# Performance work log

Hardware: AMD Instinct MI355X
Metric: run time of the kernel (lower is better)

Reference implementation:

```python
import jax, jax.numpy as jnp
import numpy as np
from jax import lax

B, C, N, NB = 64, 512, 1024, 4
BC = C // NB
KS = [3, 5, 7, 9]
LEVEL = 2  # min(2, pywt.dwt_max_level(1024, 8)) = 2
FL = 8  # db4 filter length
DN = ('NCH', 'OIH', 'NCH')
# pywt db4 decomposition filters
DEC_LO = jnp.array([-0.010597401784997278, 0.032883011666982945, 0.030841381835986965,
                    -0.18703481171888114, -0.02798376941698385, 0.6308807679295904,
                    0.7148465705525415, 0.23037781330885523], jnp.float32)
DEC_HI = jnp.array([-0.23037781330885523, 0.7148465705525415, -0.6308807679295904,
                    -0.02798376941698385, 0.18703481171888114, 0.030841381835986965,
                    -0.032883011666982945, -0.010597401784997278], jnp.float32)


def conv1d(x, w, b, pad):
    y = lax.conv_general_dilated(x, w, (1,), [(pad, pad)], dimension_numbers=DN)
    return y + b[None, :, None]


def bn_relu(x, g, beta, eps=1e-5):
    # BatchNorm1d in train mode: batch statistics over (B, L) per channel
    mu = x.mean(axis=(0, 2), keepdims=True)
    var = ((x - mu) ** 2).mean(axis=(0, 2), keepdims=True)
    xn = (x - mu) * lax.rsqrt(var + eps)
    return jax.nn.relu(xn * g[None, :, None] + beta[None, :, None])


def dwt1d(x):
    # single-level pywt-compatible DWT, symmetric mode. x: [B, C, n]
    b, c, n = x.shape
    out = (n + FL - 1) // 2
    p = 2 * (out - 1) - n + FL
    xp = jnp.pad(x, ((0, 0), (0, 0), (p // 2, p - p // 2)), mode='symmetric')
    k = jnp.stack([DEC_LO[::-1], DEC_HI[::-1]])[:, None, :]  # [2,1,FL]
    y = lax.conv_general_dilated(xp.reshape(b * c, 1, -1), k, (2,), 'VALID',
                                 dimension_numbers=DN)
    y = y.reshape(b, c, 2, out)
    return y[:, :, 0], y[:, :, 1]  # (cA, cD)


def idwt1d(lo, hi):
    # single-level inverse DWT; output length = 2*nc - FL + 2
    b, c, nc = lo.shape
    x = jnp.stack([lo, hi], axis=2).reshape(b * c, 2, nc)
    # rec filters = dec filters reversed, so flipped-for-conv == dec filters
    k = jnp.stack([DEC_LO, DEC_HI])[None, :, :]  # [1,2,FL]
    y = lax.conv_general_dilated(x, k, (1,), [(FL - 1, FL - 1)],
                                 lhs_dilation=(2,), dimension_numbers=DN)
    y = y[:, 0, FL - 2: FL - 2 + 2 * nc - FL + 2]
    return y.reshape(b, c, -1)


def decouple(x):
    # TemporalPatternDecoupling: db4 wavedec(level=2) -> reconstruct low-pass-only
    # (long term) and detail-only (short term). Torch detaches before pywt.
    x = lax.stop_gradient(x)
    n = x.shape[-1]
    a, details = x, []
    for _ in range(LEVEL):
        a, d = dwt1d(a)
        details.append(d)
    la, sa = a, jnp.zeros_like(a)
    for d in reversed(details):
        dl = d.shape[-1]
        la = idwt1d(la[..., :dl], jnp.zeros_like(d))
        sa = idwt1d(sa[..., :dl], d)
    return sa[..., :n], la[..., :n]


def setup_inputs() -> dict:
    key = jax.random.key(0)
    ks = jax.random.split(key, 32)
    s = 0.05
    inp = {
        'x': jax.random.normal(ks[0], (B, C, N), jnp.float32),
        'w_init': jax.random.normal(ks[1], (C, C, 1), jnp.float32) * s,
        'b_init': jnp.zeros((C,), jnp.float32),
        'w_pf': jax.random.normal(ks[2], (BC, 2 * BC, 1), jnp.float32) * s,
        'b_pf': jnp.zeros((BC,), jnp.float32),
        'w_fus': jax.random.normal(ks[3], (C, C, 1), jnp.float32) * s,
        'b_fus': jnp.zeros((C,), jnp.float32),
    }
    for i in range(NB):
        inp[f'w_b{i + 1}'] = jax.random.normal(ks[4 + i], (BC, BC, KS[i]), jnp.float32) * s
        inp[f'b_b{i + 1}'] = jnp.zeros((BC,), jnp.float32)
        inp[f'g_b{i + 1}'] = jnp.ones((BC,), jnp.float32)
        inp[f'be_b{i + 1}'] = jnp.zeros((BC,), jnp.float32)
    return inp


def reference(x, w_init, b_init, w_b1, b_b1, g_b1, be_b1, w_b2, b_b2, g_b2, be_b2,
              w_b3, b_b3, g_b3, be_b3, w_b4, b_b4, g_b4, be_b4, w_pf, b_pf,
              w_fus, b_fus):
    identity = x
    h = conv1d(x, w_init, b_init, 0)
    branch_in = jnp.split(h, NB, axis=1)
    wb = [w_b1, w_b2, w_b3, w_b4]
    bb = [b_b1, b_b2, b_b3, b_b4]
    gb = [g_b1, g_b2, g_b3, g_b4]
    beb = [be_b1, be_b2, be_b3, be_b4]
    shorts, longs = [], []
    for i in range(NB):
        y = bn_relu(conv1d(branch_in[i], wb[i], bb[i], KS[i] // 2), gb[i], beb[i])
        s, l = decouple(y)
        shorts.append(s)
        longs.append(l)
    for b in range(1, NB):
        shorts[b] = shorts[b] + shorts[b - 1]
    for b in range(NB - 2, -1, -1):
        longs[b] = longs[b] + longs[b + 1]
    enhanced = [conv1d(jnp.concatenate([shorts[b], longs[b]], axis=1), w_pf, b_pf, 0)
                for b in range(NB)]
    out = conv1d(jnp.concatenate(enhanced, axis=1), w_fus, b_fus, 0)
    return out + identity
```

## Files before the change

### kernel.cpp

```cpp
#include <hip/hip_runtime.h>

typedef float  f32x4 __attribute__((ext_vector_type(4)));
typedef short  s16x8 __attribute__((ext_vector_type(8)));
typedef short  s16x4 __attribute__((ext_vector_type(4)));
typedef unsigned short u16;

struct PtrQuad { const float* p[4]; };

__constant__ float c_lo[8] = {-0.010597401784997278f, 0.032883011666982945f,
                              0.030841381835986965f, -0.18703481171888114f,
                              -0.02798376941698385f, 0.6308807679295904f,
                              0.7148465705525415f,  0.23037781330885523f};
__constant__ float c_hi[8] = {-0.23037781330885523f, 0.7148465705525415f,
                              -0.6308807679295904f, -0.02798376941698385f,
                              0.18703481171888114f, 0.030841381835986965f,
                              -0.032883011666982945f, -0.010597401784997278f};

__device__ __forceinline__ u16 f2bf(float f) {
    unsigned u = __float_as_uint(f);
    u += 0x7fffu + ((u >> 16) & 1u);
    return (u16)(u >> 16);
}
__device__ __forceinline__ float bf2f(u16 h) {
    return __uint_as_float(((unsigned)h) << 16);
}
__device__ __forceinline__ int lds_chunk(int row, int g) {
    return row * 4 + (g ^ ((row >> 1) & 3));
}
__device__ __forceinline__ void gload16(void* lds, const void* g) {
    __builtin_amdgcn_global_load_lds(
        (__attribute__((address_space(1))) const void*)g,
        (__attribute__((address_space(3))) void*)lds,
        16, 0, 0);
}

__global__ __launch_bounds__(256) void gemm_nt_k(
    const u16* __restrict__ A, long aB, int lda,
    const u16* __restrict__ B, long bB, int ldb,
    int K,
    u16* __restrict__ D, long dB, int dj,
    const float* __restrict__ bias)
{
    __shared__ s16x8 As[2][512];
    __shared__ s16x8 Bs[2][512];
    const int j0 = blockIdx.x * 128, i0 = blockIdx.y * 128;
    const long bb = blockIdx.z;
    const u16* Ab = A + bb * aB;
    const u16* Bb = B + bb * bB;
    const int tid = threadIdx.x;
    const int srow = tid >> 2, sg = tid & 3;
    const int ssg = sg ^ ((srow >> 1) & 3);
    const int l = tid & 63, w = tid >> 6;
    const int wi = (w >> 1) * 64, wj = (w & 1) * 64;
    const int lr = l & 15, lg = l >> 4;
    const long aoff0 = (long)(i0 + srow) * lda + ssg * 8;
    const long aoff1 = (long)(i0 + srow + 64) * lda + ssg * 8;
    const long boff0 = (long)(j0 + srow) * ldb + ssg * 8;
    const long boff1 = (long)(j0 + srow + 64) * ldb + ssg * 8;
    const int nt = K >> 5;
    f32x4 acc[4][4] = {};
    {
        char* a0 = (char*)&As[0][0] + w * 1024;
        char* b0 = (char*)&Bs[0][0] + w * 1024;
        gload16(a0, Ab + aoff0);
        gload16(a0 + 4096, Ab + aoff1);
        gload16(b0, Bb + boff0);
        gload16(b0 + 4096, Bb + boff1);
    }
    __syncthreads();
    for (int t = 0; t < nt; ++t) {
        const int cur = t & 1;
        if (t + 1 < nt) {
            const int k0 = (t + 1) << 5;
            char* a0 = (char*)&As[cur ^ 1][0] + w * 1024;
            char* b0 = (char*)&Bs[cur ^ 1][0] + w * 1024;
            gload16(a0, Ab + aoff0 + k0);
            gload16(a0 + 4096, Ab + aoff1 + k0);
            gload16(b0, Bb + boff0 + k0);
            gload16(b0 + 4096, Bb + boff1 + k0);
        }
        s16x8 af[4], bf[4];
        #pragma unroll
        for (int f = 0; f < 4; ++f) {
            af[f] = As[cur][lds_chunk(wi + f * 16 + lr, lg)];
            bf[f] = Bs[cur][lds_chunk(wj + f * 16 + lr, lg)];
        }
        #pragma unroll
        for (int fi = 0; fi < 4; ++fi)
            #pragma unroll
            for (int fj = 0; fj < 4; ++fj)
                acc[fi][fj] = __builtin_amdgcn_mfma_f32_16x16x32_bf16(af[fi], bf[fj], acc[fi][fj], 0, 0, 0);
        __syncthreads();
    }
    u16* Db = D + bb * dB;
    #pragma unroll
    for (int fi = 0; fi < 4; ++fi) {
        const int i = i0 + wi + fi * 16 + lg * 4;
        float b0 = 0, b1 = 0, b2v = 0, b3 = 0;
        if (bias) { b0 = bias[i]; b1 = bias[i + 1]; b2v = bias[i + 2]; b3 = bias[i + 3]; }
        #pragma unroll
        for (int fj = 0; fj < 4; ++fj) {
            const int j = j0 + wj + fj * 16 + lr;
            f32x4 d = acc[fi][fj];
            s16x4 o;
            o[0] = (short)f2bf(d[0] + b0); o[1] = (short)f2bf(d[1] + b1);
            o[2] = (short)f2bf(d[2] + b2v); o[3] = (short)f2bf(d[3] + b3);
            *(s16x4*)(Db + (long)j * dj + i) = o;
        }
    }
}

__global__ __launch_bounds__(256) void gemm_branch4_k(
    const u16* __restrict__ WpAll,
    const u16* __restrict__ H,
    u16* __restrict__ Y,
    const u16* __restrict__ zbuf,
    float* __restrict__ part)
{
    __shared__ s16x8 As[2][512];
    __shared__ s16x8 Bs[2][512];
    __shared__ float sred[2][128];
    __shared__ float qred[2][128];
    const int j0 = blockIdx.x * 128;
    const int br = blockIdx.y;
    const long bb = blockIdx.z;
    const int taps = 3 + 2 * br;
    const int pad = 1 + br;
    const u16* Wp = WpAll + (long)(br * br + 2 * br) * 16384;
    const u16* Hb = H + bb * 524288 + 128 * br;
    const int tid = threadIdx.x;
    const int srow = tid >> 2, sg = tid & 3;
    const int ssg = sg ^ ((srow >> 1) & 3);
    const int l = tid & 63, w = tid >> 6;
    const int wi = (w >> 1) * 64, wj = (w & 1) * 64;
    const int lr = l & 15, lg = l >> 4;
    const int lda = taps * 128;
    const int nt = taps * 4;
    auto stage = [&](int buf, int t) {
        const int k0 = t << 5;
        const int tap = k0 >> 7, kc = k0 & 127;
        const int shift = tap - pad;
        char* a0 = (char*)&As[buf][0] + w * 1024;
        char* b0 = (char*)&Bs[buf][0] + w * 1024;
        gload16(a0, Wp + (long)srow * lda + k0 + ssg * 8);
        gload16(a0 + 4096, Wp + (long)(srow + 64) * lda + k0 + ssg * 8);
        int n0r = j0 + srow + shift;
        int n1r = n0r + 64;
        const u16* s0 = (n0r >= 0 && n0r < 1024) ? (Hb + (long)n0r * 512 + kc + ssg * 8) : zbuf;
        const u16* s1 = (n1r >= 0 && n1r < 1024) ? (Hb + (long)n1r * 512 + kc + ssg * 8) : zbuf;
        gload16(b0, s0);
        gload16(b0 + 4096, s1);
    };
    f32x4 acc[4][4] = {};
    stage(0, 0);
    __syncthreads();
    for (int t = 0; t < nt; ++t) {
        const int cur = t & 1;
        if (t + 1 < nt) stage(cur ^ 1, t + 1);
        s16x8 af[4], bf[4];
        #pragma unroll
        for (int f = 0; f < 4; ++f) {
            af[f] = As[cur][lds_chunk(wi + f * 16 + lr, lg)];
            bf[f] = Bs[cur][lds_chunk(wj + f * 16 + lr, lg)];
        }
        #pragma unroll
        for (int fi = 0; fi < 4; ++fi)
            #pragma unroll
            for (int fj = 0; fj < 4; ++fj)
                acc[fi][fj] = __builtin_amdgcn_mfma_f32_16x16x32_bf16(af[fi], bf[fj], acc[fi][fj], 0, 0, 0);
        __syncthreads();
    }
    u16* Db = Y + bb * 524288 + 128 * br;
    #pragma unroll
    for (int fi = 0; fi < 4; ++fi) {
        const int i = wi + fi * 16 + lg * 4;
        #pragma unroll
        for (int fj = 0; fj < 4; ++fj) {
            const int j = j0 + wj + fj * 16 + lr;
            f32x4 d = acc[fi][fj];
            s16x4 o;
            o[0] = (short)f2bf(d[0]); o[1] = (short)f2bf(d[1]);
            o[2] = (short)f2bf(d[2]); o[3] = (short)f2bf(d[3]);
            *(s16x4*)(Db + (long)j * 512 + i) = o;
        }
    }
    float sv[16], qv[16];
    #pragma unroll
    for (int fi = 0; fi < 4; ++fi)
        #pragma unroll
        for (int e = 0; e < 4; ++e) {
            float s = 0.f, q = 0.f;
            #pragma unroll
            for (int fj = 0; fj < 4; ++fj) { float d = acc[fi][fj][e]; s += d; q += d * d; }
            sv[fi * 4 + e] = s; qv[fi * 4 + e] = q;
        }
    #pragma unroll
    for (int m = 1; m < 16; m <<= 1) {
        #pragma unroll
        for (int r = 0; r < 16; ++r) {
            sv[r] += __shfl_xor(sv[r], m, 64);
            qv[r] += __shfl_xor(qv[r], m, 64);
        }
    }
    if (lr == 0) {
        #pragma unroll
        for (int r = 0; r < 16; ++r) {
            int co = wi + (r >> 2) * 16 + lg * 4 + (r & 3);
            sred[w & 1][co] = sv[r];
            qred[w & 1][co] = qv[r];
        }
    }
    __syncthreads();
    if (tid < 128) {
        long blk = (long)br * 512 + bb * 8 + blockIdx.x;
        part[blk * 256 + tid]       = sred[0][tid] + sred[1][tid];
        part[blk * 256 + 128 + tid] = qred[0][tid] + qred[1][tid];
    }
}

__global__ __launch_bounds__(256) void gemm_psl_k(
    const u16* __restrict__ Ybn,
    const u16* __restrict__ Bmat,
    u16* __restrict__ PSL)
{
    __shared__ s16x8 As[2][512];
    __shared__ s16x8 Bs[2][512];
    int flat = blockIdx.x + 8 * (blockIdx.y + 8 * blockIdx.z);
    int swz = (flat & 7) * 512 + (flat >> 3);
    const int j0 = (swz & 7) * 128;
    const int i0 = ((swz >> 3) & 7) * 128;
    const long bb = swz >> 6;
    const int tid = threadIdx.x;
    const u16* Ab = Ybn + bb * 524288;
    const int srow = tid >> 2, sg = tid & 3;
    const int ssg = sg ^ ((srow >> 1) & 3);
    const int l = tid & 63, w = tid >> 6;
    const int wi = (w >> 1) * 64, wj = (w & 1) * 64;
    const int lr = l & 15, lg = l >> 4;
    const long aoff0 = (long)(i0 + srow) * 512 + ssg * 8;
    const long aoff1 = (long)(i0 + srow + 64) * 512 + ssg * 8;
    const long boff0 = (long)(j0 + srow) * 512 + ssg * 8;
    const long boff1 = (long)(j0 + srow + 64) * 512 + ssg * 8;
    f32x4 acc[4][4] = {};
    {
        char* a0 = (char*)&As[0][0] + w * 1024;
        char* b0 = (char*)&Bs[0][0] + w * 1024;
        gload16(a0, Ab + aoff0);
        gload16(a0 + 4096, Ab + aoff1);
        gload16(b0, Bmat + boff0);
        gload16(b0 + 4096, Bmat + boff1);
    }
    __syncthreads();
    for (int t = 0; t < 16; ++t) {
        const int cur = t & 1;
        if (t + 1 < 16) {
            const int k0 = (t + 1) << 5;
            char* a0 = (char*)&As[cur ^ 1][0] + w * 1024;
            char* b0 = (char*)&Bs[cur ^ 1][0] + w * 1024;
            gload16(a0, Ab + aoff0 + k0);
            gload16(a0 + 4096, Ab + aoff1 + k0);
            gload16(b0, Bmat + boff0 + k0);
            gload16(b0 + 4096, Bmat + boff1 + k0);
        }
        s16x8 af[4], bf[4];
        #pragma unroll
        for (int f = 0; f < 4; ++f) {
            af[f] = As[cur][lds_chunk(wi + f * 16 + lr, lg)];
            bf[f] = Bs[cur][lds_chunk(wj + f * 16 + lr, lg)];
        }
        #pragma unroll
        for (int fi = 0; fi < 4; ++fi)
            #pragma unroll
            for (int fj = 0; fj < 4; ++fj)
                acc[fi][fj] = __builtin_amdgcn_mfma_f32_16x16x32_bf16(af[fi], bf[fj], acc[fi][fj], 0, 0, 0);
        __syncthreads();
    }
    u16* Db = PSL + bb * 1048576;
    #pragma unroll
    for (int fi = 0; fi < 4; ++fi) {
        const int i = i0 + wi + fi * 16 + lg * 4;
        #pragma unroll
        for (int fj = 0; fj < 4; ++fj) {
            const int j = j0 + wj + fj * 16 + lr;
            f32x4 d = acc[fi][fj];
            s16x4 o;
            o[0] = (short)f2bf(d[0]); o[1] = (short)f2bf(d[1]);
            o[2] = (short)f2bf(d[2]); o[3] = (short)f2bf(d[3]);
            *(s16x4*)(Db + (long)j * 1024 + i) = o;
        }
    }
}

__global__ __launch_bounds__(256) void gemm_time_k(
    const u16* __restrict__ MS, const u16* __restrict__ ML,
    const u16* __restrict__ PSL,
    const float* __restrict__ b2, const float* __restrict__ X,
    float* __restrict__ OUT)
{
    __shared__ s16x8 As[2][512];
    __shared__ s16x8 Bs[2][512];
    int flat = blockIdx.x + 4 * (blockIdx.y + 8 * blockIdx.z);
    int swz = (flat & 7) * 256 + (flat >> 3);
    const int j0 = (swz & 3) * 128;
    const int i0 = ((swz >> 2) & 7) * 128;
    const long bb = swz >> 5;
    const int tid = threadIdx.x;
    const int srow = tid >> 2, sg = tid & 3;
    const int ssg = sg ^ ((srow >> 1) & 3);
    const int l = tid & 63, w = tid >> 6;
    const int wi = (w >> 1) * 64, wj = (w & 1) * 64;
    const int lr = l & 15, lg = l >> 4;
    const int klo = (i0 - 64) > 0 ? (i0 - 64) : 0;
    const int khi = (i0 + 192) < 1024 ? (i0 + 192) : 1024;
    const int nk = (khi - klo) >> 5;
    const int nt = nk * 2;
    auto stage = [&](int buf, int t) {
        const int pass = (t >= nk) ? 1 : 0;
        const int k0 = klo + ((t - (pass ? nk : 0)) << 5);
        const u16* A = pass ? ML : MS;
        const u16* B = PSL + bb * 1048576 + (long)pass * 524288;
        char* a0 = (char*)&As[buf][0] + w * 1024;
        char* b0 = (char*)&Bs[buf][0] + w * 1024;
        gload16(a0, A + (long)(i0 + srow) * 1024 + k0 + ssg * 8);
        gload16(a0 + 4096, A + (long)(i0 + srow + 64) * 1024 + k0 + ssg * 8);
        gload16(b0, B + (long)(j0 + srow) * 1024 + k0 + ssg * 8);
        gload16(b0 + 4096, B + (long)(j0 + srow + 64) * 1024 + k0 + ssg * 8);
    };
    f32x4 acc[4][4] = {};
    stage(0, 0);
    __syncthreads();
    for (int t = 0; t < nt; ++t) {
        const int cur = t & 1;
        if (t + 1 < nt) stage(cur ^ 1, t + 1);
        s16x8 af[4], bf[4];
        #pragma unroll
        for (int f = 0; f < 4; ++f) {
            af[f] = As[cur][lds_chunk(wi + f * 16 + lr, lg)];
            bf[f] = Bs[cur][lds_chunk(wj + f * 16 + lr, lg)];
        }
        #pragma unroll
        for (int fi = 0; fi < 4; ++fi)
            #pragma unroll
            for (int fj = 0; fj < 4; ++fj)
                acc[fi][fj] = __builtin_amdgcn_mfma_f32_16x16x32_bf16(af[fi], bf[fj], acc[fi][fj], 0, 0, 0);
        __syncthreads();
    }
    float* Ob = OUT + bb * 524288;
    const float* Xb = X + bb * 524288;
    #pragma unroll
    for (int fi = 0; fi < 4; ++fi) {
        const int i = i0 + wi + fi * 16 + lg * 4;
        #pragma unroll
        for (int fj = 0; fj < 4; ++fj) {
            const int j = j0 + wj + fj * 16 + lr;
            const long a = (long)j * 1024 + i;
            f32x4 d = acc[fi][fj];
            const float bj = b2[j];
            f32x4 xv = *(const f32x4*)(Xb + a);
            f32x4 o;
            o[0] = d[0] + bj + xv[0]; o[1] = d[1] + bj + xv[1];
            o[2] = d[2] + bj + xv[2]; o[3] = d[3] + bj + xv[3];
            *(f32x4*)(Ob + a) = o;
        }
    }
}

__global__ __launch_bounds__(256) void cast_bf_k(const float* __restrict__ s, u16* __restrict__ d, int n)
{
    int i = blockIdx.x * 256 + threadIdx.x;
    if (i < n) d[i] = f2bf(s[i]);
}

__global__ __launch_bounds__(256) void pack_wb2_k(const float* __restrict__ s, u16* __restrict__ d, int taps)
{
    int i = blockIdx.x * 256 + threadIdx.x;
    if (i >= taps * 16384) return;
    int stride = taps * 128;
    int co = i / stride;
    int rem = i - co * stride;
    int tap = rem >> 7, ci = rem & 127;
    d[i] = f2bf(s[(long)(co * 128 + ci) * taps + tap]);
}

__global__ __launch_bounds__(256) void make_Ucum_k(
    const float* __restrict__ wf, const float* __restrict__ wp,
    u16* __restrict__ USc, u16* __restrict__ ULc)
{
    int gid = blockIdx.x * 256 + threadIdx.x;
    int co = gid >> 7, cc = gid & 127;
    float us[4], ul[4];
    #pragma unroll
    for (int b = 0; b < 4; ++b) {
        float s = 0.f, t = 0.f;
        for (int q = 0; q < 128; ++q) {
            float f = wf[(long)co * 512 + b * 128 + q];
            s += f * wp[q * 256 + cc];
            t += f * wp[q * 256 + 128 + cc];
        }
        us[b] = s; ul[b] = t;
    }
    float suf = 0.f;
    for (int b = 3; b >= 0; --b) { suf += us[b]; USc[(long)co * 512 + b * 128 + cc] = f2bf(suf); }
    float pre = 0.f;
    for (int b = 0; b < 4; ++b) { pre += ul[b]; ULc[(long)co * 512 + b * 128 + cc] = f2bf(pre); }
}

__global__ __launch_bounds__(256) void make_bias2_k(
    const float* __restrict__ wf, const float* __restrict__ bpf,
    const float* __restrict__ bfus, float* __restrict__ b2)
{
    int co = blockIdx.x * 256 + threadIdx.x;
    if (co >= 512) return;
    float s = bfus[co];
    for (int j = 0; j < 512; ++j) s += wf[(long)co * 512 + j] * bpf[j & 127];
    b2[co] = s;
}

__global__ __launch_bounds__(256) void eye_k(float* __restrict__ I)
{
    int i = blockIdx.x * 256 + threadIdx.x;
    I[i] = ((i >> 10) == (i & 1023)) ? 1.0f : 0.0f;
}

__global__ __launch_bounds__(256) void zero_k(float* __restrict__ p, int n)
{
    int i = blockIdx.x * 256 + threadIdx.x;
    if (i < n) p[i] = 0.f;
}

__global__ __launch_bounds__(256) void dwt_k(
    const float* __restrict__ x, float* __restrict__ a, float* __restrict__ d,
    int n_in, int n_out)
{
    const int row = blockIdx.y;
    const int m = blockIdx.x * 256 + threadIdx.x;
    if (m >= n_out) return;
    const float* xr = x + (long)row * n_in;
    float sa = 0.f, sd = 0.f;
    #pragma unroll
    for (int j = 0; j < 8; ++j) {
        int t = 2 * m + 1 - j;
        t = (t < 0) ? (-t - 1) : t;
        t = (t >= n_in) ? (2 * n_in - 1 - t) : t;
        const float v = xr[t];
        sa += v * c_lo[j];
        sd += v * c_hi[j];
    }
    a[(long)row * n_out + m] = sa;
    d[(long)row * n_out + m] = sd;
}

__global__ __launch_bounds__(256) void idwt_k(
    const float* __restrict__ lo, const float* __restrict__ hi,
    float* __restrict__ z, int nc, int n_out, long zB, int zN)
{
    const int row = blockIdx.y;
    const int m = blockIdx.x * 256 + threadIdx.x;
    if (m >= n_out) return;
    const float* lor = lo ? lo + (long)row * nc : nullptr;
    const float* hir = hi ? hi + (long)row * nc : nullptr;
    float s = 0.f;
    #pragma unroll
    for (int k = 0; k < 8; ++k) {
        int t = m + k - 1;
        if (t & 1) continue;
        int j = t >> 1;
        if (j >= nc) continue;
        if (lor) s += c_lo[k] * lor[j];
        if (hir) s += c_hi[k] * hir[j];
    }
    z[(long)(row >> 7) * zB + (long)(row & 127) * zN + m] = s;
}

__global__ __launch_bounds__(256) void trM_k(
    const float* __restrict__ S, const float* __restrict__ L,
    u16* __restrict__ MS, u16* __restrict__ ML)
{
    __shared__ float sh[32][33];
    const float* src = blockIdx.z ? L : S;
    u16* dst = blockIdx.z ? ML : MS;
    const int n0 = blockIdx.x * 32, m0 = blockIdx.y * 32;
    const int tx = threadIdx.x, ty = threadIdx.y;
    #pragma unroll
    for (int k = 0; k < 4; ++k)
        sh[ty + 8 * k][tx] = src[(long)(m0 + ty + 8 * k) * 1024 + n0 + tx];
    __syncthreads();
    #pragma unroll
    for (int k = 0; k < 4; ++k)
        dst[(long)(n0 + ty + 8 * k) * 1024 + m0 + tx] = f2bf(sh[tx][ty + 8 * k]);
}

__global__ __launch_bounds__(256) void trX_k(const float* __restrict__ x, u16* __restrict__ xcl)
{
    __shared__ float sh[32][33];
    const int n0 = blockIdx.x * 32, c0 = blockIdx.y * 32;
    const long bb = blockIdx.z;
    const int tx = threadIdx.x, ty = threadIdx.y;
    const float* xb = x + bb * 524288;
    u16* ob = xcl + bb * 524288;
    #pragma unroll
    for (int k = 0; k < 4; ++k)
        sh[ty + 8 * k][tx] = xb[(long)(c0 + ty + 8 * k) * 1024 + n0 + tx];
    __syncthreads();
    #pragma unroll
    for (int k = 0; k < 4; ++k)
        ob[(long)(n0 + ty + 8 * k) * 512 + c0 + tx] = f2bf(sh[tx][ty + 8 * k]);
}

__global__ __launch_bounds__(256) void bn_coef_k(
    const float* __restrict__ part, PtrQuad g, PtrQuad be, float* __restrict__ scsh)
{
    int c = blockIdx.x * 256 + threadIdx.x;
    if (c >= 512) return;
    int br = c >> 7, cc = c & 127;
    const float* pb = part + (long)br * 131072;
    float s = 0.f, q = 0.f;
    for (int pidx = 0; pidx < 512; ++pidx) {
        s += pb[pidx * 256 + cc];
        q += pb[pidx * 256 + 128 + cc];
    }
    float mu = s * (1.0f / 65536.0f);
    float var = q * (1.0f / 65536.0f) - mu * mu;
    float sc = g.p[br][cc] * rsqrtf(var + 1e-5f);
    scsh[c] = sc;
    scsh[512 + c] = be.p[br][cc] - mu * sc;
}

__global__ __launch_bounds__(256) void bn_apply_k(
    u16* __restrict__ Y, const float* __restrict__ scsh)
{
    __shared__ float sc_[512];
    __shared__ float sh_[512];
    const int t = threadIdx.x;
    #pragma unroll
    for (int q = 0; q < 2; ++q) {
        sc_[t + q * 256] = scsh[t + q * 256];
        sh_[t + q * 256] = scsh[512 + t + q * 256];
    }
    __syncthreads();
    long gid = (long)blockIdx.x * 256 + t;
    long r = gid >> 6; int cg = (int)(gid & 63);
    u16* p = Y + r * 512 + cg * 8;
    s16x8 v = *(const s16x8*)p;
    #pragma unroll
    for (int e = 0; e < 8; ++e) {
        int c = cg * 8 + e;
        float f = bf2f((u16)v[e]) * sc_[c] + sh_[c];
        v[e] = (short)f2bf(f > 0.f ? f : 0.f);
    }
    *(s16x8*)p = v;
}

extern "C" void kernel_launch(void* const* d_in, const int* in_sizes, int n_in,
                              void* d_out, int out_size, void* d_ws, size_t ws_size,
                              hipStream_t stream)
{
    const float* x      = (const float*)d_in[0];
    const float* w_init = (const float*)d_in[1];
    const float* b_init = (const float*)d_in[2];
    const float* w_pf   = (const float*)d_in[3];
    const float* b_pf   = (const float*)d_in[4];
    const float* w_fus  = (const float*)d_in[5];
    const float* b_fus  = (const float*)d_in[6];
    const float *w_b[4];
    PtrQuad g, be;
    for (int i = 0; i < 4; ++i) {
        w_b[i]  = (const float*)d_in[7 + 4 * i];
        g.p[i]  = (const float*)d_in[9 + 4 * i];
        be.p[i] = (const float*)d_in[10 + 4 * i];
    }
    float* outf = (float*)d_out;

    char* p = (char*)d_ws;
    u16* xcl   = (u16*)p;  p += 67108864;
    u16* h     = (u16*)p;  p += 67108864;
    u16* Y     = (u16*)p;  p += 67108864;
    u16* PSL   = (u16*)p;  p += 134217728;
    u16* Wi    = (u16*)p;  p += 524288;
    u16* Wp    = (u16*)p;  p += 786432;
    u16* UScULc= (u16*)p;  p += 1048576;
    u16* MrowS = (u16*)p;  p += 2097152;
    u16* MrowL = (u16*)p;  p += 2097152;
    float* eye = (float*)p; p += 4194304;
    float* Sid = (float*)p; p += 4194304;
    float* Lid = (float*)p; p += 4194304;
    float* a1  = (float*)p; p += 2109440;
    float* d1  = (float*)p; p += 2109440;
    float* a2  = (float*)p; p += 1069056;
    float* d2  = (float*)p; p += 1069056;
    float* la1 = (float*)p; p += 2109440;
    float* sa1 = (float*)p; p += 2109440;
    float* b2  = (float*)p; p += 2048;
    float* zbuf= (float*)p; p += 256;
    float* scsh= (float*)p; p += 4096;
    float* part= (float*)p; p += 2097152;

    const int KS_[4] = {3, 5, 7, 9};
    const long wpOff[4] = {0, 3 * 16384L, 8 * 16384L, 15 * 16384L};

    cast_bf_k<<<1024, 256, 0, stream>>>(w_init, Wi, 262144);
    for (int br = 0; br < 4; ++br)
        pack_wb2_k<<<(KS_[br] * 16384 + 255) / 256, 256, 0, stream>>>(w_b[br], Wp + wpOff[br], KS_[br]);
    make_Ucum_k<<<256, 256, 0, stream>>>(w_fus, w_pf, UScULc, UScULc + 262144);
    make_bias2_k<<<2, 256, 0, stream>>>(w_fus, b_pf, b_fus, b2);

    eye_k<<<4096, 256, 0, stream>>>(eye);
    dwt_k<<<dim3(3, 1024), 256, 0, stream>>>(eye, a1, d1, 1024, 515);
    dwt_k<<<dim3(2, 1024), 256, 0, stream>>>(a1, a2, d2, 515, 261);
    idwt_k<<<dim3(3, 1024), 256, 0, stream>>>(a2, nullptr, la1, 261, 515, 65920, 515);
    idwt_k<<<dim3(3, 1024), 256, 0, stream>>>(nullptr, d2, sa1, 261, 515, 65920, 515);
    idwt_k<<<dim3(4, 1024), 256, 0, stream>>>(la1, nullptr, Lid, 515, 1024, 131072, 1024);
    idwt_k<<<dim3(4, 1024), 256, 0, stream>>>(sa1, d1, Sid, 515, 1024, 131072, 1024);
    trM_k<<<dim3(32, 32, 2), dim3(32, 8), 0, stream>>>(Sid, Lid, MrowS, MrowL);

    trX_k<<<dim3(32, 16, 64), dim3(32, 8), 0, stream>>>(x, xcl);

    gemm_nt_k<<<dim3(8, 4, 64), 256, 0, stream>>>(Wi, 0, 512, xcl, 524288, 512, 512,
                                                  h, 524288, 512, b_init);

    zero_k<<<1, 256, 0, stream>>>(zbuf, 64);
    gemm_branch4_k<<<dim3(8, 4, 64), 256, 0, stream>>>(Wp, h, Y, (const u16*)zbuf, part);

    bn_coef_k<<<2, 256, 0, stream>>>(part, g, be, scsh);
    bn_apply_k<<<16384, 256, 0, stream>>>(Y, scsh);

    gemm_psl_k<<<dim3(8, 8, 64), 256, 0, stream>>>(Y, UScULc, PSL);

    gemm_time_k<<<dim3(4, 8, 64), 256, 0, stream>>>(MrowS, MrowL, PSL, b2, x, outf);
}
```

Measured before the change: 557.5 us.

## Triple-buffer GEMM LDS pipeline with vmcnt waits, swizzle blocks, narrow time band

Every MFMA GEMM kernel moves from a double-buffered loop to a three-stage LDS ring. Loads are issued two tiles ahead, and each step waits with explicit s_waitcnt vmcnt counts plus a raw s_barrier instead of __syncthreads, so global-to-LDS copies overlap more of the compute. The nt and branch GEMMs also get a flattened block-index swizzle to improve cache locality. The banded time GEMM's K range shrinks from ±64 to ±32 around the tile, which cuts MFMA and load work. That last change is only correct if the operator's nonzero band really fits in the narrower window, and the hardcoded swizzle assumes a fixed grid shape.

```diff
diff --git a/kernel.cpp b/kernel.cpp
--- a/kernel.cpp
+++ b/kernel.cpp
@@ -33,6 +33,17 @@
         (__attribute__((address_space(3))) void*)lds,
         16, 0, 0);
 }
+__device__ __forceinline__ void pipe_wait(int t, int nt) {
+    if (t + 2 < nt)      asm volatile("s_waitcnt vmcnt(8)" ::: "memory");
+    else if (t + 1 < nt) asm volatile("s_waitcnt vmcnt(4)" ::: "memory");
+    else                 asm volatile("s_waitcnt vmcnt(0)" ::: "memory");
+    __builtin_amdgcn_s_barrier();
+    __builtin_amdgcn_sched_barrier(0);
+}
+__device__ __forceinline__ void pipe_endbar() {
+    __builtin_amdgcn_sched_barrier(0);
+    __builtin_amdgcn_s_barrier();
+}
 
 __global__ __launch_bounds__(256) void gemm_nt_k(
     const u16* __restrict__ A, long aB, int lda,
@@ -41,10 +52,13 @@
     u16* __restrict__ D, long dB, int dj,
     const float* __restrict__ bias)
 {
-    __shared__ s16x8 As[2][512];
-    __shared__ s16x8 Bs[2][512];
-    const int j0 = blockIdx.x * 128, i0 = blockIdx.y * 128;
-    const long bb = blockIdx.z;
+    __shared__ s16x8 As[3 * 512];
+    __shared__ s16x8 Bs[3 * 512];
+    int flat = blockIdx.x + 8 * (blockIdx.y + 4 * blockIdx.z);
+    int swz = (flat & 7) * 256 + (flat >> 3);
+    const int j0 = (swz & 7) * 128;
+    const int i0 = ((swz >> 3) & 3) * 128;
+    const long bb = swz >> 5;
     const u16* Ab = A + bb * aB;
     const u16* Bb = B + bb * bB;
     const int tid = threadIdx.x;
@@ -58,39 +72,35 @@
     const long boff0 = (long)(j0 + srow) * ldb + ssg * 8;
     const long boff1 = (long)(j0 + srow + 64) * ldb + ssg * 8;
     const int nt = K >> 5;
+    auto stage = [&](int buf, int t) {
+        const int k0 = t << 5;
+        char* a0 = (char*)As + buf * 8192 + w * 1024;
+        char* b0 = (char*)Bs + buf * 8192 + w * 1024;
+        gload16(a0, Ab + aoff0 + k0);
+        gload16(a0 + 4096, Ab + aoff1 + k0);
+        gload16(b0, Bb + boff0 + k0);
+        gload16(b0 + 4096, Bb + boff1 + k0);
+    };
     f32x4 acc[4][4] = {};
-    {
-        char* a0 = (char*)&As[0][0] + w * 1024;
-        char* b0 = (char*)&Bs[0][0] + w * 1024;
-        gload16(a0, Ab + aoff0);
-        gload16(a0 + 4096, Ab + aoff1);
-        gload16(b0, Bb + boff0);
-        gload16(b0 + 4096, Bb + boff1);
-    }
-    __syncthreads();
+    stage(0, 0);
+    if (nt > 1) stage(1, 1);
+    int cur = 0;
     for (int t = 0; t < nt; ++t) {
-        const int cur = t & 1;
-        if (t + 1 < nt) {
-            const int k0 = (t + 1) << 5;
-            char* a0 = (char*)&As[cur ^ 1][0] + w * 1024;
-            char* b0 = (char*)&Bs[cur ^ 1][0] + w * 1024;
-            gload16(a0, Ab + aoff0 + k0);
-            gload16(a0 + 4096, Ab + aoff1 + k0);
-            gload16(b0, Bb + boff0 + k0);
-            gload16(b0 + 4096, Bb + boff1 + k0);
-        }
+        if (t + 2 < nt) stage((cur + 2) % 3, t + 2);
+        pipe_wait(t, nt);
         s16x8 af[4], bf[4];
         #pragma unroll
         for (int f = 0; f < 4; ++f) {
-            af[f] = As[cur][lds_chunk(wi + f * 16 + lr, lg)];
-            bf[f] = Bs[cur][lds_chunk(wj + f * 16 + lr, lg)];
+            af[f] = As[cur * 512 + lds_chunk(wi + f * 16 + lr, lg)];
+            bf[f] = Bs[cur * 512 + lds_chunk(wj + f * 16 + lr, lg)];
         }
         #pragma unroll
         for (int fi = 0; fi < 4; ++fi)
             #pragma unroll
             for (int fj = 0; fj < 4; ++fj)
                 acc[fi][fj] = __builtin_amdgcn_mfma_f32_16x16x32_bf16(af[fi], bf[fj], acc[fi][fj], 0, 0, 0);
-        __syncthreads();
+        pipe_endbar();
+        cur = (cur + 1) % 3;
     }
     u16* Db = D + bb * dB;
     #pragma unroll
@@ -117,13 +127,16 @@
     const u16* __restrict__ zbuf,
     float* __restrict__ part)
 {
-    __shared__ s16x8 As[2][512];
-    __shared__ s16x8 Bs[2][512];
+    __shared__ s16x8 As[3 * 512];
+    __shared__ s16x8 Bs[3 * 512];
     __shared__ float sred[2][128];
     __shared__ float qred[2][128];
-    const int j0 = blockIdx.x * 128;
-    const int br = blockIdx.y;
-    const long bb = blockIdx.z;
+    int flat = blockIdx.x + 8 * (blockIdx.y + 4 * blockIdx.z);
+    int swz = (flat & 7) * 256 + (flat >> 3);
+    const int jblk = swz & 7;
+    const int br = (swz >> 3) & 3;
+    const long bb = swz >> 5;
+    const int j0 = jblk * 128;
     const int taps = 3 + 2 * br;
     const int pad = 1 + br;
     const u16* Wp = WpAll + (long)(br * br + 2 * br) * 16384;
@@ -140,8 +153,8 @@
         const int k0 = t << 5;
         const int tap = k0 >> 7, kc = k0 & 127;
         const int shift = tap - pad;
-        char* a0 = (char*)&As[buf][0] + w * 1024;
-        char* b0 = (char*)&Bs[buf][0] + w * 1024;
+        char* a0 = (char*)As + buf * 8192 + w * 1024;
+        char* b0 = (char*)Bs + buf * 8192 + w * 1024;
         gload16(a0, Wp + (long)srow * lda + k0 + ssg * 8);
         gload16(a0 + 4096, Wp + (long)(srow + 64) * lda + k0 + ssg * 8);
         int n0r = j0 + srow + shift;
@@ -153,22 +166,24 @@
     };
     f32x4 acc[4][4] = {};
     stage(0, 0);
-    __syncthreads();
+    stage(1, 1);
+    int cur = 0;
     for (int t = 0; t < nt; ++t) {
-        const int cur = t & 1;
-        if (t + 1 < nt) stage(cur ^ 1, t + 1);
+        if (t + 2 < nt) stage((cur + 2) % 3, t + 2);
+        pipe_wait(t, nt);
         s16x8 af[4], bf[4];
         #pragma unroll
         for (int f = 0; f < 4; ++f) {
-            af[f] = As[cur][lds_chunk(wi + f * 16 + lr, lg)];
-            bf[f] = Bs[cur][lds_chunk(wj + f * 16 + lr, lg)];
+            af[f] = As[cur * 512 + lds_chunk(wi + f * 16 + lr, lg)];
+            bf[f] = Bs[cur * 512 + lds_chunk(wj + f * 16 + lr, lg)];
         }
         #pragma unroll
         for (int fi = 0; fi < 4; ++fi)
             #pragma unroll
             for (int fj = 0; fj < 4; ++fj)
                 acc[fi][fj] = __builtin_amdgcn_mfma_f32_16x16x32_bf16(af[fi], bf[fj], acc[fi][fj], 0, 0, 0);
-        __syncthreads();
+        pipe_endbar();
+        cur = (cur + 1) % 3;
     }
     u16* Db = Y + bb * 524288 + 128 * br;
     #pragma unroll
@@ -202,6 +217,7 @@
             qv[r] += __shfl_xor(qv[r], m, 64);
         }
     }
+    __syncthreads();
     if (lr == 0) {
         #pragma unroll
         for (int r = 0; r < 16; ++r) {
@@ -212,7 +228,7 @@
     }
     __syncthreads();
     if (tid < 128) {
-        long blk = (long)br * 512 + bb * 8 + blockIdx.x;
+        long blk = (long)br * 512 + bb * 8 + jblk;
         part[blk * 256 + tid]       = sred[0][tid] + sred[1][tid];
         part[blk * 256 + 128 + tid] = qred[0][tid] + qred[1][tid];
     }
@@ -223,8 +239,8 @@
     const u16* __restrict__ Bmat,
     u16* __restrict__ PSL)
 {
-    __shared__ s16x8 As[2][512];
-    __shared__ s16x8 Bs[2][512];
+    __shared__ s16x8 As[3 * 512];
+    __shared__ s16x8 Bs[3 * 512];
     int flat = blockIdx.x + 8 * (blockIdx.y + 8 * blockIdx.z);
     int swz = (flat & 7) * 512 + (flat >> 3);
     const int j0 = (swz & 7) * 128;
@@ -241,39 +257,36 @@
     const long aoff1 = (long)(i0 + srow + 64) * 512 + ssg * 8;
     const long boff0 = (long)(j0 + srow) * 512 + ssg * 8;
     const long boff1 = (long)(j0 + srow + 64) * 512 + ssg * 8;
+    const int nt = 16;
+    auto stage = [&](int buf, int t) {
+        const int k0 = t << 5;
+        char* a0 = (char*)As + buf * 8192 + w * 1024;
+        char* b0 = (char*)Bs + buf * 8192 + w * 1024;
+        gload16(a0, Ab + aoff0 + k0);
+        gload16(a0 + 4096, Ab + aoff1 + k0);
+        gload16(b0, Bmat + boff0 + k0);
+        gload16(b0 + 4096, Bmat + boff1 + k0);
+    };
     f32x4 acc[4][4] = {};
-    {
-        char* a0 = (char*)&As[0][0] + w * 1024;
-        char* b0 = (char*)&Bs[0][0] + w * 1024;
-        gload16(a0, Ab + aoff0);
-        gload16(a0 + 4096, Ab + aoff1);
-        gload16(b0, Bmat + boff0);
-        gload16(b0 + 4096, Bmat + boff1);
-    }
-    __syncthreads();
-    for (int t = 0; t < 16; ++t) {
-        const int cur = t & 1;
-        if (t + 1 < 16) {
-            const int k0 = (t + 1) << 5;
-            char* a0 = (char*)&As[cur ^ 1][0] + w * 1024;
-            char* b0 = (char*)&Bs[cur ^ 1][0] + w * 1024;
-            gload16(a0, Ab + aoff0 + k0);
-            gload16(a0 + 4096, Ab + aoff1 + k0);
-            gload16(b0, Bmat + boff0 + k0);
-            gload16(b0 + 4096, Bmat + boff1 + k0);
-        }
+    stage(0, 0);
+    stage(1, 1);
+    int cur = 0;
+    for (int t = 0; t < nt; ++t) {
+        if (t + 2 < nt) stage((cur + 2) % 3, t + 2);
+        pipe_wait(t, nt);
         s16x8 af[4], bf[4];
         #pragma unroll
         for (int f = 0; f < 4; ++f) {
-            af[f] = As[cur][lds_chunk(wi + f * 16 + lr, lg)];
-            bf[f] = Bs[cur][lds_chunk(wj + f * 16 + lr, lg)];
+            af[f] = As[cur * 512 + lds_chunk(wi + f * 16 + lr, lg)];
+            bf[f] = Bs[cur * 512 + lds_chunk(wj + f * 16 + lr, lg)];
         }
         #pragma unroll
         for (int fi = 0; fi < 4; ++fi)
             #pragma unroll
             for (int fj = 0; fj < 4; ++fj)
                 acc[fi][fj] = __builtin_amdgcn_mfma_f32_16x16x32_bf16(af[fi], bf[fj], acc[fi][fj], 0, 0, 0);
-        __syncthreads();
+        pipe_endbar();
+        cur = (cur + 1) % 3;
     }
     u16* Db = PSL + bb * 1048576;
     #pragma unroll
@@ -297,8 +310,8 @@
     const float* __restrict__ b2, const float* __restrict__ X,
     float* __restrict__ OUT)
 {
-    __shared__ s16x8 As[2][512];
-    __shared__ s16x8 Bs[2][512];
+    __shared__ s16x8 As[3 * 512];
+    __shared__ s16x8 Bs[3 * 512];
     int flat = blockIdx.x + 4 * (blockIdx.y + 8 * blockIdx.z);
     int swz = (flat & 7) * 256 + (flat >> 3);
     const int j0 = (swz & 3) * 128;
@@ -310,8 +323,8 @@
     const int l = tid & 63, w = tid >> 6;
     const int wi = (w >> 1) * 64, wj = (w & 1) * 64;
     const int lr = l & 15, lg = l >> 4;
-    const int klo = (i0 - 64) > 0 ? (i0 - 64) : 0;
-    const int khi = (i0 + 192) < 1024 ? (i0 + 192) : 1024;
+    const int klo = (i0 - 32) > 0 ? (i0 - 32) : 0;
+    const int khi = (i0 + 160) < 1024 ? (i0 + 160) : 1024;
     const int nk = (khi - klo) >> 5;
     const int nt = nk * 2;
     auto stage = [&](int buf, int t) {
@@ -319,8 +332,8 @@
         const int k0 = klo + ((t - (pass ? nk : 0)) << 5);
         const u16* A = pass ? ML : MS;
         const u16* B = PSL + bb * 1048576 + (long)pass * 524288;
-        char* a0 = (char*)&As[buf][0] + w * 1024;
-        char* b0 = (char*)&Bs[buf][0] + w * 1024;
+        char* a0 = (char*)As + buf * 8192 + w * 1024;
+        char* b0 = (char*)Bs + buf * 8192 + w * 1024;
         gload16(a0, A + (long)(i0 + srow) * 1024 + k0 + ssg * 8);
         gload16(a0 + 4096, A + (long)(i0 + srow + 64) * 1024 + k0 + ssg * 8);
         gload16(b0, B + (long)(j0 + srow) * 1024 + k0 + ssg * 8);
@@ -328,22 +341,24 @@
     };
     f32x4 acc[4][4] = {};
     stage(0, 0);
-    __syncthreads();
+    stage(1, 1);
+    int cur = 0;
     for (int t = 0; t < nt; ++t) {
-        const int cur = t & 1;
-        if (t + 1 < nt) stage(cur ^ 1, t + 1);
+        if (t + 2 < nt) stage((cur + 2) % 3, t + 2);
+        pipe_wait(t, nt);
         s16x8 af[4], bf[4];
         #pragma unroll
         for (int f = 0; f < 4; ++f) {
-            af[f] = As[cur][lds_chunk(wi + f * 16 + lr, lg)];
-            bf[f] = Bs[cur][lds_chunk(wj + f * 16 + lr, lg)];
+            af[f] = As[cur * 512 + lds_chunk(wi + f * 16 + lr, lg)];
+            bf[f] = Bs[cur * 512 + lds_chunk(wj + f * 16 + lr, lg)];
         }
         #pragma unroll
         for (int fi = 0; fi < 4; ++fi)
             #pragma unroll
             for (int fj = 0; fj < 4; ++fj)
                 acc[fi][fj] = __builtin_amdgcn_mfma_f32_16x16x32_bf16(af[fi], bf[fj], acc[fi][fj], 0, 0, 0);
-        __syncthreads();
+        pipe_endbar();
+        cur = (cur + 1) % 3;
     }
     float* Ob = OUT + bb * 524288;
     const float* Xb = X + bb * 524288;
```

Result: faster. 539.4 us (-3.3%).
